# Performance work log

Hardware: AMD Instinct MI355X
Metric: run time of the kernel (lower is better)

Reference implementation:

```python
import jax, jax.numpy as jnp
import numpy as np

SHAPES = [(100, 100), (50, 50), (25, 25), (13, 13)]
N_HEADS, N_LEVELS, N_POINTS, D_MODEL, D_FFN = 8, 4, 4, 256, 1024
HEAD_DIM = D_MODEL // N_HEADS
S_TOTAL = sum(h * w for h, w in SHAPES)
BATCH = 2


def _layernorm(x, g, b, eps=1e-5):
    m = jnp.mean(x, -1, keepdims=True)
    v = jnp.mean((x - m) ** 2, -1, keepdims=True)
    return (x - m) * jax.lax.rsqrt(v + eps) * g + b


def _bilinear_sample(value_l, loc, Hl, Wl):
    # value_l: (N, Hl, Wl, nh, hd); loc: (N, Lq, nh, P, 2) normalized to [0,1]
    # Matches torch grid_sample(mode='bilinear', padding_mode='zeros', align_corners=False)
    x = loc[..., 0] * Wl - 0.5
    y = loc[..., 1] * Hl - 0.5
    x0 = jnp.floor(x); y0 = jnp.floor(y)
    wx1 = x - x0; wx0 = 1.0 - wx1
    wy1 = y - y0; wy0 = 1.0 - wy1
    x0i = x0.astype(jnp.int32); x1i = x0i + 1
    y0i = y0.astype(jnp.int32); y1i = y0i + 1
    N, Lq, nh, P = x.shape
    n_idx = jnp.arange(N)[:, None, None, None]
    h_idx = jnp.arange(nh)[None, None, :, None]

    def gather(yi, xi):
        valid = (yi >= 0) & (yi < Hl) & (xi >= 0) & (xi < Wl)
        yc = jnp.clip(yi, 0, Hl - 1); xc = jnp.clip(xi, 0, Wl - 1)
        v = value_l[n_idx, yc, xc, h_idx]  # (N, Lq, nh, P, hd)
        return v * valid[..., None].astype(v.dtype)

    return (gather(y0i, x0i) * (wy0 * wx0)[..., None]
            + gather(y0i, x1i) * (wy0 * wx1)[..., None]
            + gather(y1i, x0i) * (wy1 * wx0)[..., None]
            + gather(y1i, x1i) * (wy1 * wx1)[..., None])


def _forward(src, pos, reference_points, W_off, b_off, W_attn, b_attn, W_val, b_val,
             W_out, b_out, W1, b1, W2, b2, g1, beta1, g2, beta2):
    N, S, C = src.shape
    q = src + pos  # with_pos_embed
    # MSDeformAttn
    off = (q @ W_off + b_off).reshape(N, S, N_HEADS, N_LEVELS, N_POINTS, 2)
    aw = jax.nn.softmax((q @ W_attn + b_attn).reshape(N, S, N_HEADS, N_LEVELS * N_POINTS), axis=-1)
    aw = aw.reshape(N, S, N_HEADS, N_LEVELS, N_POINTS)
    value = (src @ W_val + b_val).reshape(N, S, N_HEADS, HEAD_DIM)
    # offset normalizer is (W_l, H_l) per level
    normalizer = jnp.array([[wl, hl] for hl, wl in SHAPES], dtype=src.dtype)  # (L, 2)
    loc = reference_points[:, :, None, :, None, :] + off / normalizer[None, None, None, :, None, :]
    out = jnp.zeros((N, S, N_HEADS, HEAD_DIM), src.dtype)
    start = 0
    for l, (Hl, Wl) in enumerate(SHAPES):
        v_l = value[:, start:start + Hl * Wl].reshape(N, Hl, Wl, N_HEADS, HEAD_DIM)
        sampled = _bilinear_sample(v_l, loc[:, :, :, l], Hl, Wl)  # (N,S,nh,P,hd)
        out = out + jnp.einsum('nqhp,nqhpd->nqhd', aw[:, :, :, l], sampled)
        start += Hl * Wl
    src2 = out.reshape(N, S, C) @ W_out + b_out
    # residual + norm1 (dropout is identity in eval)
    x = _layernorm(src + src2, g1, beta1)
    # FFN + residual + norm2
    ff = jax.nn.relu(x @ W1 + b1) @ W2 + b2
    return _layernorm(x + ff, g2, beta2)


def setup_inputs() -> dict:
    key = jax.random.key(0)
    ks = jax.random.split(key, 16)
    f32 = jnp.float32

    def w(k, shape, scale=0.02):
        return jax.random.normal(k, shape, dtype=f32) * scale

    return {
        "src": jax.random.normal(ks[0], (BATCH, S_TOTAL, D_MODEL), dtype=f32),
        "pos": jax.random.normal(ks[1], (BATCH, S_TOTAL, D_MODEL), dtype=f32),
        "reference_points": jax.random.uniform(ks[2], (BATCH, S_TOTAL, N_LEVELS, 2), dtype=f32),
        "spatial_shapes": jnp.array(SHAPES, dtype=jnp.int32),
        "level_start_index": jnp.array(np.cumsum([0] + [h * w for h, w in SHAPES[:-1]]), dtype=jnp.int32),
        "W_off": w(ks[3], (D_MODEL, N_HEADS * N_LEVELS * N_POINTS * 2)),
        "b_off": w(ks[4], (N_HEADS * N_LEVELS * N_POINTS * 2,), 0.5),
        "W_attn": w(ks[5], (D_MODEL, N_HEADS * N_LEVELS * N_POINTS)),
        "b_attn": w(ks[6], (N_HEADS * N_LEVELS * N_POINTS,)),
        "W_val": w(ks[7], (D_MODEL, D_MODEL)),
        "b_val": w(ks[8], (D_MODEL,)),
        "W_out": w(ks[9], (D_MODEL, D_MODEL)),
        "b_out": w(ks[10], (D_MODEL,)),
        "W1": w(ks[11], (D_MODEL, D_FFN)),
        "b1": w(ks[12], (D_FFN,)),
        "W2": w(ks[13], (D_FFN, D_MODEL)),
        "b2": w(ks[14], (D_MODEL,)),
        "g1": jnp.ones((D_MODEL,), f32),
        "beta1": jnp.zeros((D_MODEL,), f32),
        "g2": jnp.ones((D_MODEL,), f32),
        "beta2": jnp.zeros((D_MODEL,), f32),
    }


def reference(src, pos, reference_points, spatial_shapes, level_start_index,
              W_off, b_off, W_attn, b_attn, W_val, b_val, W_out, b_out,
              W1, b1, W2, b2, g1, beta1, g2, beta2):
    # spatial_shapes / level_start_index are static metadata mirrored by SHAPES
    return _forward(src, pos, reference_points, W_off, b_off, W_attn, b_attn,
                    W_val, b_val, W_out, b_out, W1, b1, W2, b2, g1, beta1, g2, beta2)
```

## Files before the change

### kernel.cpp

```cpp
#include <hip/hip_runtime.h>


typedef __bf16 bf16x8 __attribute__((ext_vector_type(8)));
typedef __bf16 bf16x4 __attribute__((ext_vector_type(4)));
typedef float floatx4 __attribute__((ext_vector_type(4)));

#define S_TOTAL 13294
#define M_ROWS  26588
#define M_PAD   26624

#define MFMA16(a, b, c) __builtin_amdgcn_mfma_f32_16x16x32_bf16(a, b, c, 0, 0, 0)

__global__ __launch_bounds__(256) void cvt_k(
    const float* __restrict__ Woff, const float* __restrict__ Wattn,
    const float* __restrict__ Wval, const float* __restrict__ Wout,
    const float* __restrict__ W1,   const float* __restrict__ W2,
    const float* __restrict__ boff, const float* __restrict__ battn,
    __bf16* __restrict__ wbase, float* __restrict__ bc) {
    int b = blockIdx.x;
    if (b >= 184) {
        for (int i = threadIdx.x; i < 384; i += 256)
            bc[i] = (i < 256) ? boff[i] : battn[i - 256];
        return;
    }
    const float* W; __bf16* D; int K, N, t;
    if (b < 16)       { W = Woff;  D = wbase;          K = 256;  N = 256;  t = b; }
    else if (b < 24)  { W = Wattn; D = wbase + 65536;  K = 256;  N = 128;  t = b - 16; }
    else if (b < 40)  { W = Wval;  D = wbase + 98304;  K = 256;  N = 256;  t = b - 24; }
    else if (b < 56)  { W = Wout;  D = wbase + 163840; K = 256;  N = 256;  t = b - 40; }
    else if (b < 120) { W = W1;    D = wbase + 229376; K = 256;  N = 1024; t = b - 56; }
    else              { W = W2;    D = wbase + 491520; K = 1024; N = 256;  t = b - 120; }
    int tk = K >> 6;
    int n0 = (t / tk) << 6, k0 = (t % tk) << 6;
    __shared__ float T[64][65];
    int tid = threadIdx.x;
    int rr = tid >> 4, cc = (tid & 15) << 2;
#pragma unroll
    for (int p = 0; p < 4; p++) {
        int r = p * 16 + rr;
        float4 v = *(const float4*)(W + (size_t)(k0 + r) * N + n0 + cc);
        T[r][cc] = v.x; T[r][cc + 1] = v.y; T[r][cc + 2] = v.z; T[r][cc + 3] = v.w;
    }
    __syncthreads();
#pragma unroll
    for (int p = 0; p < 4; p++) {
        int n = p * 16 + rr;
        bf16x4 o = {(__bf16)T[cc][n], (__bf16)T[cc + 1][n],
                    (__bf16)T[cc + 2][n], (__bf16)T[cc + 3][n]};
        *(bf16x4*)(D + (size_t)(n0 + n) * K + k0 + cc) = o;
    }
}

template <int J, bool SUMPOS, bool BF16OUT>
__global__ __launch_bounds__(512, 4) void gemm_src(
    const float* __restrict__ Af, const float* __restrict__ Pf,
    const __bf16* __restrict__ BT, const float* __restrict__ bias,
    float* __restrict__ Cf, __bf16* __restrict__ Cb, int N) {
    constexpr int ASTR = 264;
    __shared__ __align__(16) __bf16 As[32 * ASTR];
    const int tid = threadIdx.x, wave = tid >> 6, lane = tid & 63;
    const int l16 = lane & 15, quad = lane >> 4;
    const int row0 = blockIdx.x * 32;
#pragma unroll
    for (int p = 0; p < 4; p++) {
        int fe = (p * 512 + tid) * 4;
        int m = fe >> 8, k = fe & 255;
        int row = min(row0 + m, M_ROWS - 1);
        float4 s = *(const float4*)(Af + (size_t)row * 256 + k);
        if (SUMPOS) {
            float4 pp = *(const float4*)(Pf + (size_t)row * 256 + k);
            s.x += pp.x; s.y += pp.y; s.z += pp.z; s.w += pp.w;
        }
        bf16x4 v = {(__bf16)s.x, (__bf16)s.y, (__bf16)s.z, (__bf16)s.w};
        *(bf16x4*)(As + m * ASTR + k) = v;
    }
    __syncthreads();
    const int n0 = wave * (J * 16);
    floatx4 acc[2][J] = {};
    bf16x8 bb[2][J];
#pragma unroll
    for (int j = 0; j < J; j++)
        bb[0][j] = *(const bf16x8*)(BT + (size_t)(n0 + j * 16 + l16) * 256 + quad * 8);
#pragma unroll
    for (int ki = 0; ki < 8; ki++) {
        const int cur = ki & 1;
        if (ki < 7) {
#pragma unroll
            for (int j = 0; j < J; j++)
                bb[cur ^ 1][j] = *(const bf16x8*)(BT + (size_t)(n0 + j * 16 + l16) * 256
                                                  + (ki + 1) * 32 + quad * 8);
        }
        bf16x8 af[2];
#pragma unroll
        for (int i = 0; i < 2; i++)
            af[i] = *(const bf16x8*)(As + (i * 16 + l16) * ASTR + ki * 32 + quad * 8);
#pragma unroll
        for (int i = 0; i < 2; i++)
#pragma unroll
            for (int j = 0; j < J; j++)
                acc[i][j] = MFMA16(af[i], bb[cur][j], acc[i][j]);
    }
    float bv[J];
#pragma unroll
    for (int j = 0; j < J; j++) bv[j] = bias[n0 + j * 16 + l16];
#pragma unroll
    for (int i = 0; i < 2; i++)
#pragma unroll
        for (int j = 0; j < J; j++)
#pragma unroll
            for (int r = 0; r < 4; r++) {
                float v = acc[i][j][r] + bv[j];
                size_t gi = (size_t)(row0 + i * 16 + quad * 4 + r) * N + n0 + j * 16 + l16;
                if (BF16OUT) Cb[gi] = (__bf16)v;
                else         Cf[gi] = v;
            }
}

__global__ __launch_bounds__(256) void sample_k(const float* __restrict__ offa,
                                                const __bf16* __restrict__ valb,
                                                const float* __restrict__ refp,
                                                __bf16* __restrict__ outb) {
    const int r   = blockIdx.x;
    const int tid = threadIdx.x;
    if (r >= M_ROWS) {
        outb[(size_t)r * 256 + tid] = (__bf16)0.f;
        return;
    }
    __shared__ float2 s_wo[4][128];
    const int n = (r >= S_TOTAL) ? 1 : 0;

    if (tid < 128) {
        const int HLc[4] = {100, 50, 25, 13};
        const int STc[4] = {0, 10000, 12500, 13125};
        int lp = tid & 15, l = lp >> 2;
        float logit = offa[(size_t)r * 384 + 256 + tid];
        float mx = logit;
        mx = fmaxf(mx, __shfl_xor(mx, 1));
        mx = fmaxf(mx, __shfl_xor(mx, 2));
        mx = fmaxf(mx, __shfl_xor(mx, 4));
        mx = fmaxf(mx, __shfl_xor(mx, 8));
        float e = __expf(logit - mx);
        float s = e;
        s += __shfl_xor(s, 1); s += __shfl_xor(s, 2);
        s += __shfl_xor(s, 4); s += __shfl_xor(s, 8);
        float aw = e / s;

        float2 o2 = *(const float2*)(offa + (size_t)r * 384 + tid * 2);
        float rx = refp[((size_t)r * 4 + l) * 2];
        float ry = refp[((size_t)r * 4 + l) * 2 + 1];
        int   Wl = HLc[l];
        float x = rx * (float)Wl + o2.x - 0.5f;
        float y = ry * (float)Wl + o2.y - 0.5f;
        float xf = floorf(x), yf = floorf(y);
        float wx1 = x - xf, wy1 = y - yf;
        float wx0 = 1.f - wx1, wy0 = 1.f - wy1;
        int x0 = (int)xf, y0 = (int)yf;
        int base = n * S_TOTAL + STc[l];
#pragma unroll
        for (int c = 0; c < 4; c++) {
            int yy = y0 + (c >> 1), xx = x0 + (c & 1);
            bool valid = (yy >= 0) & (yy < Wl) & (xx >= 0) & (xx < Wl);
            int yc = min(max(yy, 0), Wl - 1);
            int xc = min(max(xx, 0), Wl - 1);
            float w = ((c >> 1) ? wy1 : wy0) * ((c & 1) ? wx1 : wx0);
            int off = (base + yc * Wl + xc) * 512;
            s_wo[c][tid] = make_float2(valid ? w * aw : 0.f, __int_as_float(off));
        }
    }
    __syncthreads();

    const int h  = tid >> 5;
    const int pg = (tid >> 2) & 7;
    const int cg = tid & 3;
    const char* vbase = (const char*)valb + h * 64 + cg * 16;
    float a[8] = {};
#pragma unroll
    for (int pp = 0; pp < 2; pp++) {
        int idx = h * 16 + pg * 2 + pp;
#pragma unroll
        for (int c = 0; c < 4; c++) {
            float2 wo = s_wo[c][idx];
            float  w  = wo.x;
            bf16x8 v  = *(const bf16x8*)(vbase + __float_as_int(wo.y));
#pragma unroll
            for (int k = 0; k < 8; k++) a[k] += w * (float)v[k];
        }
    }
#pragma unroll
    for (int k = 0; k < 8; k++) {
        a[k] += __shfl_xor(a[k], 4);
        a[k] += __shfl_xor(a[k], 8);
        a[k] += __shfl_xor(a[k], 16);
    }
    if (pg == 0) {
        bf16x8 res;
#pragma unroll
        for (int k = 0; k < 8; k++) res[k] = (__bf16)a[k];
        *(bf16x8*)(outb + (size_t)r * 256 + h * 32 + cg * 8) = res;
    }
}

__global__ __launch_bounds__(512, 4) void oln_k(
    const __bf16* __restrict__ A, const __bf16* __restrict__ BT,
    const float* __restrict__ bias, const float* __restrict__ src,
    const float* __restrict__ g, const float* __restrict__ be,
    float* __restrict__ x, __bf16* __restrict__ xb) {
    constexpr int ASTR = 264;
    __shared__ __align__(16) __bf16 As[32 * ASTR];
    __shared__ float rs[32], rq[32];
    const int tid = threadIdx.x, wave = tid >> 6, lane = tid & 63;
    const int l16 = lane & 15, quad = lane >> 4;
    const int row0 = blockIdx.x * 32;
#pragma unroll
    for (int p = 0; p < 2; p++) {
        int fg = p * 512 + tid;
        int m = fg >> 5, gg = fg & 31;
        *(bf16x8*)(As + m * ASTR + gg * 8) =
            *(const bf16x8*)(A + (size_t)(row0 + m) * 256 + gg * 8);
    }
    if (tid < 32) { rs[tid] = 0.f; rq[tid] = 0.f; }
    __syncthreads();
    const int n0 = wave * 32;
    floatx4 acc[2][2] = {};
    bf16x8 bb[2][2];
#pragma unroll
    for (int j = 0; j < 2; j++)
        bb[0][j] = *(const bf16x8*)(BT + (size_t)(n0 + j * 16 + l16) * 256 + quad * 8);
#pragma unroll
    for (int ki = 0; ki < 8; ki++) {
        const int cur = ki & 1;
        if (ki < 7) {
#pragma unroll
            for (int j = 0; j < 2; j++)
                bb[cur ^ 1][j] = *(const bf16x8*)(BT + (size_t)(n0 + j * 16 + l16) * 256
                                                  + (ki + 1) * 32 + quad * 8);
        }
        bf16x8 af[2];
#pragma unroll
        for (int i = 0; i < 2; i++)
            af[i] = *(const bf16x8*)(As + (i * 16 + l16) * ASTR + ki * 32 + quad * 8);
#pragma unroll
        for (int i = 0; i < 2; i++)
#pragma unroll
            for (int j = 0; j < 2; j++)
                acc[i][j] = MFMA16(af[i], bb[cur][j], acc[i][j]);
    }
    float bv[2], gv[2], bev[2];
#pragma unroll
    for (int j = 0; j < 2; j++) {
        bv[j]  = bias[n0 + j * 16 + l16];
        gv[j]  = g[n0 + j * 16 + l16];
        bev[j] = be[n0 + j * 16 + l16];
    }
    float vals[2][2][4];
#pragma unroll
    for (int i = 0; i < 2; i++)
#pragma unroll
        for (int r = 0; r < 4; r++) {
            int lrow = i * 16 + quad * 4 + r;
            int rowc = min(row0 + lrow, M_ROWS - 1);
            float s = 0.f, q = 0.f;
#pragma unroll
            for (int j = 0; j < 2; j++) {
                float v = acc[i][j][r] + bv[j]
                        + src[(size_t)rowc * 256 + n0 + j * 16 + l16];
                vals[i][j][r] = v;
                s += v; q += v * v;
            }
            s += __shfl_xor(s, 1); s += __shfl_xor(s, 2);
            s += __shfl_xor(s, 4); s += __shfl_xor(s, 8);
            q += __shfl_xor(q, 1); q += __shfl_xor(q, 2);
            q += __shfl_xor(q, 4); q += __shfl_xor(q, 8);
            if (l16 == 0) { atomicAdd(&rs[lrow], s); atomicAdd(&rq[lrow], q); }
        }
    __syncthreads();
#pragma unroll
    for (int i = 0; i < 2; i++)
#pragma unroll
        for (int r = 0; r < 4; r++) {
            int lrow = i * 16 + quad * 4 + r;
            float mean = rs[lrow] * (1.f / 256.f);
            float var  = rq[lrow] * (1.f / 256.f) - mean * mean;
            float rstd = rsqrtf(var + 1e-5f);
#pragma unroll
            for (int j = 0; j < 2; j++) {
                float o = (vals[i][j][r] - mean) * rstd * gv[j] + bev[j];
                size_t gi = (size_t)(row0 + lrow) * 256 + n0 + j * 16 + l16;
                x[gi]  = o;
                xb[gi] = (__bf16)o;
            }
        }
}

__global__ __launch_bounds__(512, 4) void ffn_k(
    const __bf16* __restrict__ xb, const __bf16* __restrict__ W1T,
    const __bf16* __restrict__ W2T, const float* __restrict__ b1,
    const float* __restrict__ b2, const float* __restrict__ x,
    const float* __restrict__ g, const float* __restrict__ be,
    float* __restrict__ out) {
    constexpr int ASTR = 264, HSTR = 264;
    __shared__ __align__(16) __bf16 As[32 * ASTR];
    __shared__ __align__(16) __bf16 Hs[32 * HSTR];
    __shared__ float rs[32], rq[32];
    const int tid = threadIdx.x, wave = tid >> 6, lane = tid & 63;
    const int l16 = lane & 15, quad = lane >> 4;
    const int row0 = blockIdx.x * 32;
#pragma unroll
    for (int p = 0; p < 2; p++) {
        int fg = p * 512 + tid;
        int m = fg >> 5, gg = fg & 31;
        *(bf16x8*)(As + m * ASTR + gg * 8) =
            *(const bf16x8*)(xb + (size_t)(row0 + m) * 256 + gg * 8);
    }
    if (tid < 32) { rs[tid] = 0.f; rq[tid] = 0.f; }
    __syncthreads();

    float b1v[4][2];
#pragma unroll
    for (int hc = 0; hc < 4; hc++)
#pragma unroll
        for (int j = 0; j < 2; j++)
            b1v[hc][j] = b1[hc * 256 + wave * 32 + j * 16 + l16];

    floatx4 facc[2][2] = {};
#pragma unroll
    for (int hc = 0; hc < 4; hc++) {
        floatx4 hacc[2][2] = {};
        {
            bf16x8 wb[2][2];
#pragma unroll
            for (int j = 0; j < 2; j++)
                wb[0][j] = *(const bf16x8*)(W1T
                    + (size_t)(hc * 256 + wave * 32 + j * 16 + l16) * 256 + quad * 8);
#pragma unroll
            for (int ki = 0; ki < 8; ki++) {
                const int cur = ki & 1;
                if (ki < 7) {
#pragma unroll
                    for (int j = 0; j < 2; j++)
                        wb[cur ^ 1][j] = *(const bf16x8*)(W1T
                            + (size_t)(hc * 256 + wave * 32 + j * 16 + l16) * 256
                            + (ki + 1) * 32 + quad * 8);
                }
                bf16x8 af[2];
#pragma unroll
                for (int i = 0; i < 2; i++)
                    af[i] = *(const bf16x8*)(As + (i * 16 + l16) * ASTR + ki * 32 + quad * 8);
#pragma unroll
                for (int i = 0; i < 2; i++)
#pragma unroll
                    for (int j = 0; j < 2; j++)
                        hacc[i][j] = MFMA16(af[i], wb[cur][j], hacc[i][j]);
            }
        }
        __syncthreads();
#pragma unroll
        for (int i = 0; i < 2; i++)
#pragma unroll
            for (int j = 0; j < 2; j++)
#pragma unroll
                for (int r = 0; r < 4; r++)
                    Hs[(i * 16 + quad * 4 + r) * HSTR + wave * 32 + j * 16 + l16] =
                        (__bf16)fmaxf(hacc[i][j][r] + b1v[hc][j], 0.f);
        __syncthreads();
        {
            bf16x8 wb[2][2];
#pragma unroll
            for (int j = 0; j < 2; j++)
                wb[0][j] = *(const bf16x8*)(W2T
                    + (size_t)(wave * 32 + j * 16 + l16) * 1024 + hc * 256 + quad * 8);
#pragma unroll
            for (int ki = 0; ki < 8; ki++) {
                const int cur = ki & 1;
                if (ki < 7) {
#pragma unroll
                    for (int j = 0; j < 2; j++)
                        wb[cur ^ 1][j] = *(const bf16x8*)(W2T
                            + (size_t)(wave * 32 + j * 16 + l16) * 1024
                            + hc * 256 + (ki + 1) * 32 + quad * 8);
                }
                bf16x8 ah[2];
#pragma unroll
                for (int i = 0; i < 2; i++)
                    ah[i] = *(const bf16x8*)(Hs + (i * 16 + l16) * HSTR + ki * 32 + quad * 8);
#pragma unroll
                for (int i = 0; i < 2; i++)
#pragma unroll
                    for (int j = 0; j < 2; j++)
                        facc[i][j] = MFMA16(ah[i], wb[cur][j], facc[i][j]);
            }
        }
    }
    const int n0 = wave * 32;
    float b2v[2], gv[2], bev[2];
#pragma unroll
    for (int j = 0; j < 2; j++) {
        b2v[j] = b2[n0 + j * 16 + l16];
        gv[j]  = g[n0 + j * 16 + l16];
        bev[j] = be[n0 + j * 16 + l16];
    }
    float vals[2][2][4];
#pragma unroll
    for (int i = 0; i < 2; i++)
#pragma unroll
        for (int r = 0; r < 4; r++) {
            int lrow = i * 16 + quad * 4 + r;
            float s = 0.f, q = 0.f;
#pragma unroll
            for (int j = 0; j < 2; j++) {
                float v = facc[i][j][r] + b2v[j]
                        + x[(size_t)(row0 + lrow) * 256 + n0 + j * 16 + l16];
                vals[i][j][r] = v;
                s += v; q += v * v;
            }
            s += __shfl_xor(s, 1); s += __shfl_xor(s, 2);
            s += __shfl_xor(s, 4); s += __shfl_xor(s, 8);
            q += __shfl_xor(q, 1); q += __shfl_xor(q, 2);
            q += __shfl_xor(q, 4); q += __shfl_xor(q, 8);
            if (l16 == 0) { atomicAdd(&rs[lrow], s); atomicAdd(&rq[lrow], q); }
        }
    __syncthreads();
#pragma unroll
    for (int i = 0; i < 2; i++)
#pragma unroll
        for (int r = 0; r < 4; r++) {
            int lrow = i * 16 + quad * 4 + r;
            int row  = row0 + lrow;
            if (row < M_ROWS) {
                float mean = rs[lrow] * (1.f / 256.f);
                float var  = rq[lrow] * (1.f / 256.f) - mean * mean;
                float rstd = rsqrtf(var + 1e-5f);
#pragma unroll
                for (int j = 0; j < 2; j++) {
                    float o = (vals[i][j][r] - mean) * rstd * gv[j] + bev[j];
                    out[(size_t)row * 256 + n0 + j * 16 + l16] = o;
                }
            }
        }
}

extern "C" void kernel_launch(void* const* d_in, const int* in_sizes, int n_in,
                              void* d_out, int out_size, void* d_ws, size_t ws_size,
                              hipStream_t stream) {
    const float* src  = (const float*)d_in[0];
    const float* pos  = (const float*)d_in[1];
    const float* refp = (const float*)d_in[2];
    const float* W_off  = (const float*)d_in[5];
    const float* b_off  = (const float*)d_in[6];
    const float* W_attn = (const float*)d_in[7];
    const float* b_attn = (const float*)d_in[8];
    const float* W_val  = (const float*)d_in[9];
    const float* b_val  = (const float*)d_in[10];
    const float* W_out  = (const float*)d_in[11];
    const float* b_out  = (const float*)d_in[12];
    const float* W1     = (const float*)d_in[13];
    const float* b1     = (const float*)d_in[14];
    const float* W2     = (const float*)d_in[15];
    const float* b2     = (const float*)d_in[16];
    const float* g1     = (const float*)d_in[17];
    const float* beta1  = (const float*)d_in[18];
    const float* g2     = (const float*)d_in[19];
    const float* beta2  = (const float*)d_in[20];
    float* out = (float*)d_out;

    const size_t RB = (size_t)M_PAD * 256 * 2;
    const size_t RF = (size_t)M_PAD * 256 * 4;
    char* ws = (char*)d_ws;
    __bf16* outb = (__bf16*)(ws);
    __bf16* valb = (__bf16*)(ws + RB);
    float*  offa = (float*)(ws + 2 * RB);
    float*  x    = (float*)(ws + 2 * RB);
    __bf16* xb   = (__bf16*)(ws + 2 * RB + RF);
    char*   regW = ws + 2 * RB + (size_t)M_PAD * 384 * 4;

    __bf16* WTcomb = (__bf16*)regW;
    __bf16* WTval  = (__bf16*)(regW + 196608);
    __bf16* WTout  = (__bf16*)(regW + 327680);
    __bf16* WT1    = (__bf16*)(regW + 458752);
    __bf16* WT2    = (__bf16*)(regW + 983040);
    float*  bc     = (float*)(regW + 1507328);

    cvt_k<<<185, 256, 0, stream>>>(W_off, W_attn, W_val, W_out, W1, W2,
                                   b_off, b_attn, WTcomb, bc);

    gemm_src<3, true, false><<<832, 512, 0, stream>>>(
        src, pos, WTcomb, bc, offa, nullptr, 384);
    gemm_src<2, false, true><<<832, 512, 0, stream>>>(
        src, src, WTval, b_val, nullptr, valb, 256);

    sample_k<<<M_PAD, 256, 0, stream>>>(offa, valb, refp, outb);

    oln_k<<<832, 512, 0, stream>>>(outb, WTout, b_out, src, g1, beta1, x, xb);

    ffn_k<<<832, 512, 0, stream>>>(xb, WT1, WT2, b1, b2, x, g2, beta2, out);
}
```

Baseline: 390.6 us.

## Enlarge GEMM row tiles to 128 with XOR-swizzled LDS and restructured FFN

All four GEMM-style kernels now process 128 rows per block instead of 32, using dynamic shared memory with an XOR swizzle in place of padded strides. Each weight fragment loaded from global memory is therefore reused across four times as many rows. The FFN kernel is reorganised into two wave groups of 64 rows that walk the hidden dimension in 128-wide chunks, with 64 output columns per wave. In exchange the grid shrinks to 208 blocks, which is below the CU count, and larger LDS and register footprints cut occupancy.

```diff
diff --git a/kernel.cpp b/kernel.cpp
--- a/kernel.cpp
+++ b/kernel.cpp
@@ -10,6 +10,8 @@
 #define M_PAD   26624
 
 #define MFMA16(a, b, c) __builtin_amdgcn_mfma_f32_16x16x32_bf16(a, b, c, 0, 0, 0)
+#define SWA(m, g) ((m) * 256 + ((((g) ^ ((m) & 31))) << 3))
+#define SWH(r, g) ((r) * 128 + ((((g) ^ ((r) & 15))) << 3))
 
 __global__ __launch_bounds__(256) void cvt_k(
     const float* __restrict__ Woff, const float* __restrict__ Wattn,
@@ -52,31 +54,37 @@
 }
 
 template <int J, bool SUMPOS, bool BF16OUT>
-__global__ __launch_bounds__(512, 4) void gemm_src(
+__global__ __launch_bounds__(512, 2) void gemm_src(
     const float* __restrict__ Af, const float* __restrict__ Pf,
     const __bf16* __restrict__ BT, const float* __restrict__ bias,
     float* __restrict__ Cf, __bf16* __restrict__ Cb, int N) {
-    constexpr int ASTR = 264;
-    __shared__ __align__(16) __bf16 As[32 * ASTR];
+    extern __shared__ __align__(16) char smem[];
+    __bf16* As = (__bf16*)smem;
     const int tid = threadIdx.x, wave = tid >> 6, lane = tid & 63;
     const int l16 = lane & 15, quad = lane >> 4;
-    const int row0 = blockIdx.x * 32;
-#pragma unroll
-    for (int p = 0; p < 4; p++) {
-        int fe = (p * 512 + tid) * 4;
-        int m = fe >> 8, k = fe & 255;
+    const int row0 = blockIdx.x * 128;
+#pragma unroll
+    for (int p = 0; p < 8; p++) {
+        int fg = p * 512 + tid;
+        int m = fg >> 5, gn = fg & 31;
         int row = min(row0 + m, M_ROWS - 1);
-        float4 s = *(const float4*)(Af + (size_t)row * 256 + k);
+        const float* sp = Af + (size_t)row * 256 + gn * 8;
+        float4 a0 = *(const float4*)sp;
+        float4 a1 = *(const float4*)(sp + 4);
         if (SUMPOS) {
-            float4 pp = *(const float4*)(Pf + (size_t)row * 256 + k);
-            s.x += pp.x; s.y += pp.y; s.z += pp.z; s.w += pp.w;
-        }
-        bf16x4 v = {(__bf16)s.x, (__bf16)s.y, (__bf16)s.z, (__bf16)s.w};
-        *(bf16x4*)(As + m * ASTR + k) = v;
+            const float* pp = Pf + (size_t)row * 256 + gn * 8;
+            float4 p0 = *(const float4*)pp;
+            float4 p1 = *(const float4*)(pp + 4);
+            a0.x += p0.x; a0.y += p0.y; a0.z += p0.z; a0.w += p0.w;
+            a1.x += p1.x; a1.y += p1.y; a1.z += p1.z; a1.w += p1.w;
+        }
+        bf16x8 v = {(__bf16)a0.x, (__bf16)a0.y, (__bf16)a0.z, (__bf16)a0.w,
+                    (__bf16)a1.x, (__bf16)a1.y, (__bf16)a1.z, (__bf16)a1.w};
+        *(bf16x8*)(As + SWA(m, gn)) = v;
     }
     __syncthreads();
     const int n0 = wave * (J * 16);
-    floatx4 acc[2][J] = {};
+    floatx4 acc[8][J] = {};
     bf16x8 bb[2][J];
 #pragma unroll
     for (int j = 0; j < J; j++)
@@ -90,21 +98,20 @@
                 bb[cur ^ 1][j] = *(const bf16x8*)(BT + (size_t)(n0 + j * 16 + l16) * 256
                                                   + (ki + 1) * 32 + quad * 8);
         }
-        bf16x8 af[2];
-#pragma unroll
-        for (int i = 0; i < 2; i++)
-            af[i] = *(const bf16x8*)(As + (i * 16 + l16) * ASTR + ki * 32 + quad * 8);
-#pragma unroll
-        for (int i = 0; i < 2; i++)
+#pragma unroll
+        for (int i = 0; i < 8; i++) {
+            int m = i * 16 + l16;
+            bf16x8 af = *(const bf16x8*)(As + SWA(m, ki * 4 + quad));
 #pragma unroll
             for (int j = 0; j < J; j++)
-                acc[i][j] = MFMA16(af[i], bb[cur][j], acc[i][j]);
+                acc[i][j] = MFMA16(af, bb[cur][j], acc[i][j]);
+        }
     }
     float bv[J];
 #pragma unroll
     for (int j = 0; j < J; j++) bv[j] = bias[n0 + j * 16 + l16];
 #pragma unroll
-    for (int i = 0; i < 2; i++)
+    for (int i = 0; i < 8; i++)
 #pragma unroll
         for (int j = 0; j < J; j++)
 #pragma unroll
@@ -200,28 +207,29 @@
     }
 }
 
-__global__ __launch_bounds__(512, 4) void oln_k(
+__global__ __launch_bounds__(512, 2) void oln_k(
     const __bf16* __restrict__ A, const __bf16* __restrict__ BT,
     const float* __restrict__ bias, const float* __restrict__ src,
     const float* __restrict__ g, const float* __restrict__ be,
     float* __restrict__ x, __bf16* __restrict__ xb) {
-    constexpr int ASTR = 264;
-    __shared__ __align__(16) __bf16 As[32 * ASTR];
-    __shared__ float rs[32], rq[32];
+    extern __shared__ __align__(16) char smem[];
+    __bf16* As = (__bf16*)smem;
+    float*  rs = (float*)(smem + 65536);
+    float*  rq = rs + 128;
     const int tid = threadIdx.x, wave = tid >> 6, lane = tid & 63;
     const int l16 = lane & 15, quad = lane >> 4;
-    const int row0 = blockIdx.x * 32;
-#pragma unroll
-    for (int p = 0; p < 2; p++) {
+    const int row0 = blockIdx.x * 128;
+#pragma unroll
+    for (int p = 0; p < 8; p++) {
         int fg = p * 512 + tid;
-        int m = fg >> 5, gg = fg & 31;
-        *(bf16x8*)(As + m * ASTR + gg * 8) =
-            *(const bf16x8*)(A + (size_t)(row0 + m) * 256 + gg * 8);
-    }
-    if (tid < 32) { rs[tid] = 0.f; rq[tid] = 0.f; }
+        int m = fg >> 5, gn = fg & 31;
+        *(bf16x8*)(As + SWA(m, gn)) =
+            *(const bf16x8*)(A + (size_t)(row0 + m) * 256 + gn * 8);
+    }
+    if (tid < 128) { rs[tid] = 0.f; rq[tid] = 0.f; }
     __syncthreads();
     const int n0 = wave * 32;
-    floatx4 acc[2][2] = {};
+    floatx4 acc[8][2] = {};
     bf16x8 bb[2][2];
 #pragma unroll
     for (int j = 0; j < 2; j++)
@@ -235,15 +243,14 @@
                 bb[cur ^ 1][j] = *(const bf16x8*)(BT + (size_t)(n0 + j * 16 + l16) * 256
                                                   + (ki + 1) * 32 + quad * 8);
         }
-        bf16x8 af[2];
-#pragma unroll
-        for (int i = 0; i < 2; i++)
-            af[i] = *(const bf16x8*)(As + (i * 16 + l16) * ASTR + ki * 32 + quad * 8);
-#pragma unroll
-        for (int i = 0; i < 2; i++)
+#pragma unroll
+        for (int i = 0; i < 8; i++) {
+            int m = i * 16 + l16;
+            bf16x8 af = *(const bf16x8*)(As + SWA(m, ki * 4 + quad));
 #pragma unroll
             for (int j = 0; j < 2; j++)
-                acc[i][j] = MFMA16(af[i], bb[cur][j], acc[i][j]);
+                acc[i][j] = MFMA16(af, bb[cur][j], acc[i][j]);
+        }
     }
     float bv[2], gv[2], bev[2];
 #pragma unroll
@@ -252,9 +259,9 @@
         gv[j]  = g[n0 + j * 16 + l16];
         bev[j] = be[n0 + j * 16 + l16];
     }
-    float vals[2][2][4];
-#pragma unroll
-    for (int i = 0; i < 2; i++)
+    float vals[8][2][4];
+#pragma unroll
+    for (int i = 0; i < 8; i++)
 #pragma unroll
         for (int r = 0; r < 4; r++) {
             int lrow = i * 16 + quad * 4 + r;
@@ -275,7 +282,7 @@
         }
     __syncthreads();
 #pragma unroll
-    for (int i = 0; i < 2; i++)
+    for (int i = 0; i < 8; i++)
 #pragma unroll
         for (int r = 0; r < 4; r++) {
             int lrow = i * 16 + quad * 4 + r;
@@ -292,122 +299,117 @@
         }
 }
 
-__global__ __launch_bounds__(512, 4) void ffn_k(
+__global__ __launch_bounds__(512, 2) void ffn_k(
     const __bf16* __restrict__ xb, const __bf16* __restrict__ W1T,
     const __bf16* __restrict__ W2T, const float* __restrict__ b1,
     const float* __restrict__ b2, const float* __restrict__ x,
     const float* __restrict__ g, const float* __restrict__ be,
     float* __restrict__ out) {
-    constexpr int ASTR = 264, HSTR = 264;
-    __shared__ __align__(16) __bf16 As[32 * ASTR];
-    __shared__ __align__(16) __bf16 Hs[32 * HSTR];
-    __shared__ float rs[32], rq[32];
+    extern __shared__ __align__(16) char smem[];
+    __bf16* As = (__bf16*)smem;
+    __bf16* Hs = (__bf16*)(smem + 65536);
+    float*  rs = (float*)(smem + 98304);
+    float*  rq = rs + 128;
     const int tid = threadIdx.x, wave = tid >> 6, lane = tid & 63;
     const int l16 = lane & 15, quad = lane >> 4;
-    const int row0 = blockIdx.x * 32;
-#pragma unroll
-    for (int p = 0; p < 2; p++) {
+    const int grp = wave >> 2;
+    const int wq  = wave & 3;
+    const int row0 = blockIdx.x * 128;
+#pragma unroll
+    for (int p = 0; p < 8; p++) {
         int fg = p * 512 + tid;
-        int m = fg >> 5, gg = fg & 31;
-        *(bf16x8*)(As + m * ASTR + gg * 8) =
-            *(const bf16x8*)(xb + (size_t)(row0 + m) * 256 + gg * 8);
-    }
-    if (tid < 32) { rs[tid] = 0.f; rq[tid] = 0.f; }
-    __syncthreads();
-
-    float b1v[4][2];
-#pragma unroll
-    for (int hc = 0; hc < 4; hc++)
+        int m = fg >> 5, gn = fg & 31;
+        *(bf16x8*)(As + SWA(m, gn)) =
+            *(const bf16x8*)(xb + (size_t)(row0 + m) * 256 + gn * 8);
+    }
+    if (tid < 128) { rs[tid] = 0.f; rq[tid] = 0.f; }
+    __syncthreads();
+
+    floatx4 facc[4][4] = {};
+    for (int ch = 0; ch < 8; ch++) {
+        const int hc0 = ch * 128 + wq * 32;
+        floatx4 hacc[4][2] = {};
+        bf16x8 wb[2][2];
 #pragma unroll
         for (int j = 0; j < 2; j++)
-            b1v[hc][j] = b1[hc * 256 + wave * 32 + j * 16 + l16];
-
-    floatx4 facc[2][2] = {};
-#pragma unroll
-    for (int hc = 0; hc < 4; hc++) {
-        floatx4 hacc[2][2] = {};
-        {
-            bf16x8 wb[2][2];
+            wb[0][j] = *(const bf16x8*)(W1T + (size_t)(hc0 + j * 16 + l16) * 256 + quad * 8);
+#pragma unroll
+        for (int ki = 0; ki < 8; ki++) {
+            const int cur = ki & 1;
+            if (ki < 7) {
+#pragma unroll
+                for (int j = 0; j < 2; j++)
+                    wb[cur ^ 1][j] = *(const bf16x8*)(W1T
+                        + (size_t)(hc0 + j * 16 + l16) * 256 + (ki + 1) * 32 + quad * 8);
+            }
+#pragma unroll
+            for (int i = 0; i < 4; i++) {
+                int m = grp * 64 + i * 16 + l16;
+                bf16x8 af = *(const bf16x8*)(As + SWA(m, ki * 4 + quad));
+#pragma unroll
+                for (int j = 0; j < 2; j++)
+                    hacc[i][j] = MFMA16(af, wb[cur][j], hacc[i][j]);
+            }
+        }
+        __syncthreads();
+        float b1v[2];
+#pragma unroll
+        for (int j = 0; j < 2; j++) b1v[j] = b1[hc0 + j * 16 + l16];
+#pragma unroll
+        for (int i = 0; i < 4; i++)
 #pragma unroll
             for (int j = 0; j < 2; j++)
-                wb[0][j] = *(const bf16x8*)(W1T
-                    + (size_t)(hc * 256 + wave * 32 + j * 16 + l16) * 256 + quad * 8);
-#pragma unroll
-            for (int ki = 0; ki < 8; ki++) {
-                const int cur = ki & 1;
-                if (ki < 7) {
-#pragma unroll
-                    for (int j = 0; j < 2; j++)
-                        wb[cur ^ 1][j] = *(const bf16x8*)(W1T
-                            + (size_t)(hc * 256 + wave * 32 + j * 16 + l16) * 256
-                            + (ki + 1) * 32 + quad * 8);
+#pragma unroll
+                for (int r = 0; r < 4; r++) {
+                    int rr = grp * 64 + i * 16 + quad * 4 + r;
+                    int cc = wq * 32 + j * 16 + l16;
+                    Hs[SWH(rr, cc >> 3) + (cc & 7)] =
+                        (__bf16)fmaxf(hacc[i][j][r] + b1v[j], 0.f);
                 }
-                bf16x8 af[2];
-#pragma unroll
-                for (int i = 0; i < 2; i++)
-                    af[i] = *(const bf16x8*)(As + (i * 16 + l16) * ASTR + ki * 32 + quad * 8);
-#pragma unroll
-                for (int i = 0; i < 2; i++)
-#pragma unroll
-                    for (int j = 0; j < 2; j++)
-                        hacc[i][j] = MFMA16(af[i], wb[cur][j], hacc[i][j]);
-            }
-        }
         __syncthreads();
-#pragma unroll
-        for (int i = 0; i < 2; i++)
-#pragma unroll
-            for (int j = 0; j < 2; j++)
-#pragma unroll
-                for (int r = 0; r < 4; r++)
-                    Hs[(i * 16 + quad * 4 + r) * HSTR + wave * 32 + j * 16 + l16] =
-                        (__bf16)fmaxf(hacc[i][j][r] + b1v[hc][j], 0.f);
-        __syncthreads();
-        {
-            bf16x8 wb[2][2];
-#pragma unroll
-            for (int j = 0; j < 2; j++)
-                wb[0][j] = *(const bf16x8*)(W2T
-                    + (size_t)(wave * 32 + j * 16 + l16) * 1024 + hc * 256 + quad * 8);
-#pragma unroll
-            for (int ki = 0; ki < 8; ki++) {
-                const int cur = ki & 1;
-                if (ki < 7) {
-#pragma unroll
-                    for (int j = 0; j < 2; j++)
-                        wb[cur ^ 1][j] = *(const bf16x8*)(W2T
-                            + (size_t)(wave * 32 + j * 16 + l16) * 1024
-                            + hc * 256 + (ki + 1) * 32 + quad * 8);
-                }
-                bf16x8 ah[2];
-#pragma unroll
-                for (int i = 0; i < 2; i++)
-                    ah[i] = *(const bf16x8*)(Hs + (i * 16 + l16) * HSTR + ki * 32 + quad * 8);
-#pragma unroll
-                for (int i = 0; i < 2; i++)
-#pragma unroll
-                    for (int j = 0; j < 2; j++)
-                        facc[i][j] = MFMA16(ah[i], wb[cur][j], facc[i][j]);
-            }
-        }
-    }
-    const int n0 = wave * 32;
-    float b2v[2], gv[2], bev[2];
-#pragma unroll
-    for (int j = 0; j < 2; j++) {
+        const int n0 = wq * 64;
+        bf16x8 vb[2][4];
+#pragma unroll
+        for (int j = 0; j < 4; j++)
+            vb[0][j] = *(const bf16x8*)(W2T + (size_t)(n0 + j * 16 + l16) * 1024
+                                        + ch * 128 + quad * 8);
+#pragma unroll
+        for (int ki = 0; ki < 4; ki++) {
+            const int cur = ki & 1;
+            if (ki < 3) {
+#pragma unroll
+                for (int j = 0; j < 4; j++)
+                    vb[cur ^ 1][j] = *(const bf16x8*)(W2T
+                        + (size_t)(n0 + j * 16 + l16) * 1024
+                        + ch * 128 + (ki + 1) * 32 + quad * 8);
+            }
+#pragma unroll
+            for (int i = 0; i < 4; i++) {
+                int rr = grp * 64 + i * 16 + l16;
+                bf16x8 ah = *(const bf16x8*)(Hs + SWH(rr, ki * 4 + quad));
+#pragma unroll
+                for (int j = 0; j < 4; j++)
+                    facc[i][j] = MFMA16(ah, vb[cur][j], facc[i][j]);
+            }
+        }
+    }
+    const int n0 = wq * 64;
+    float b2v[4], gv[4], bev[4];
+#pragma unroll
+    for (int j = 0; j < 4; j++) {
         b2v[j] = b2[n0 + j * 16 + l16];
         gv[j]  = g[n0 + j * 16 + l16];
         bev[j] = be[n0 + j * 16 + l16];
     }
-    float vals[2][2][4];
-#pragma unroll
-    for (int i = 0; i < 2; i++)
+    float vals[4][4][4];
+#pragma unroll
+    for (int i = 0; i < 4; i++)
 #pragma unroll
         for (int r = 0; r < 4; r++) {
-            int lrow = i * 16 + quad * 4 + r;
+            int lrow = grp * 64 + i * 16 + quad * 4 + r;
             float s = 0.f, q = 0.f;
 #pragma unroll
-            for (int j = 0; j < 2; j++) {
+            for (int j = 0; j < 4; j++) {
                 float v = facc[i][j][r] + b2v[j]
                         + x[(size_t)(row0 + lrow) * 256 + n0 + j * 16 + l16];
                 vals[i][j][r] = v;
@@ -421,17 +423,17 @@
         }
     __syncthreads();
 #pragma unroll
-    for (int i = 0; i < 2; i++)
+    for (int i = 0; i < 4; i++)
 #pragma unroll
         for (int r = 0; r < 4; r++) {
-            int lrow = i * 16 + quad * 4 + r;
+            int lrow = grp * 64 + i * 16 + quad * 4 + r;
             int row  = row0 + lrow;
             if (row < M_ROWS) {
                 float mean = rs[lrow] * (1.f / 256.f);
                 float var  = rq[lrow] * (1.f / 256.f) - mean * mean;
                 float rstd = rsqrtf(var + 1e-5f);
 #pragma unroll
-                for (int j = 0; j < 2; j++) {
+                for (int j = 0; j < 4; j++) {
                     float o = (vals[i][j][r] - mean) * rstd * gv[j] + bev[j];
                     out[(size_t)row * 256 + n0 + j * 16 + l16] = o;
                 }
@@ -483,14 +485,14 @@
     cvt_k<<<185, 256, 0, stream>>>(W_off, W_attn, W_val, W_out, W1, W2,
                                    b_off, b_attn, WTcomb, bc);
 
-    gemm_src<3, true, false><<<832, 512, 0, stream>>>(
+    gemm_src<3, true, false><<<208, 512, 65536, stream>>>(
         src, pos, WTcomb, bc, offa, nullptr, 384);
-    gemm_src<2, false, true><<<832, 512, 0, stream>>>(
+    gemm_src<2, false, true><<<208, 512, 65536, stream>>>(
         src, src, WTval, b_val, nullptr, valb, 256);
 
     sample_k<<<M_PAD, 256, 0, stream>>>(offa, valb, refp, outb);
 
-    oln_k<<<832, 512, 0, stream>>>(outb, WTout, b_out, src, g1, beta1, x, xb);
-
-    ffn_k<<<832, 512, 0, stream>>>(xb, WT1, WT2, b1, b2, x, g2, beta2, out);
-}
+    oln_k<<<208, 512, 66560, stream>>>(outb, WTout, b_out, src, g1, beta1, x, xb);
+
+    ffn_k<<<208, 512, 99328, stream>>>(xb, WT1, WT2, b1, b2, x, g2, beta2, out);
+}
```

After: 325.9 us. 16.6% less time.
